# Kernel optimization log

Hardware: AMD Instinct MI355X
Metric: run time of the kernel (lower is better)

The kernel has to match this reference:

```python
import jax, jax.numpy as jnp
import numpy as np

PQ_M = 8
VALS_PER_DIM = 256
SUB_DIM = 64
EMB = PQ_M * SUB_DIM  # 512
NUM_ITEMS = 1_000_000
BATCH = 256
SEQ = 512


def setup_inputs() -> dict:
    key = jax.random.key(0)
    k1, k2, k3 = jax.random.split(key, 3)
    input_ids = jax.random.randint(k1, (BATCH, SEQ), 0, NUM_ITEMS, dtype=jnp.int64 if jax.config.jax_enable_x64 else jnp.int32).astype(jnp.int32)
    item_codes = jax.random.randint(k2, (NUM_ITEMS, PQ_M), 0, VALS_PER_DIM, dtype=jnp.int32)
    centroids = jax.random.normal(k3, (PQ_M, VALS_PER_DIM, SUB_DIM), dtype=jnp.float32)
    # module zeroes centroid index 0 in every subspace at init
    centroids = centroids.at[:, 0, :].set(0.0)
    return {"input_ids": input_ids, "item_codes": item_codes, "centroids": centroids}


def reference(input_ids, item_codes, centroids):
    # input_ids: [B, S] int; item_codes: [N, M] int32; centroids: [M, V, D] f32
    codes = item_codes[input_ids]                       # [B, S, M]
    codes = jnp.minimum(codes, VALS_PER_DIM - 1)        # clamp per subspace
    byte_idx = jnp.arange(PQ_M, dtype=jnp.int32)        # [M]
    # per-subspace gather: centroids[m, codes[b,s,m]] -> [B, S, M, D]
    sub = centroids[byte_idx[None, None, :], codes]
    B, S = input_ids.shape
    result = sub.reshape(B, S, EMB)                     # concat subspaces
    pad = (input_ids == 0)[:, :, None]                  # zero padding tokens
    return jnp.where(pad, 0.0, result)
```

## Files before the change

kernel.cpp:

```cpp
#include <hip/hip_runtime.h>


#define PQ_M_ 8
#define VALS_ 256
#define SUB_ 64
#define NTOK_ (256 * 512)
#define TOK_PER_BLK 64
#define THREADS 256

typedef float f4 __attribute__((ext_vector_type(4)));

__global__ __launch_bounds__(THREADS) void ItemCode_kernel(
    const int* __restrict__ input_ids,
    const int* __restrict__ item_codes,
    const float* __restrict__ centroids,
    float* __restrict__ out)
{
    __shared__ int s_cidx[TOK_PER_BLK * PQ_M_];

    const int tok_base = blockIdx.x * TOK_PER_BLK;

    #pragma unroll
    for (int k = threadIdx.x; k < TOK_PER_BLK * PQ_M_; k += THREADS) {
        const int t  = k >> 3;
        const int m  = k & 7;
        const int id = input_ids[tok_base + t];
        int code = 0;
        if (id != 0) {
            code = __builtin_nontemporal_load(&item_codes[id * PQ_M_ + m]);
            code = min(code, VALS_ - 1);
        }
        s_cidx[k] = ((m * VALS_) + code) << 4;
    }
    __syncthreads();

    const f4* __restrict__ cent4 = reinterpret_cast<const f4*>(centroids);
    f4* __restrict__ out4 = reinterpret_cast<f4*>(out);
    const int out_base = tok_base * 128;

    #pragma unroll 8
    for (int i = threadIdx.x; i < TOK_PER_BLK * 128; i += THREADS) {
        const int t   = i >> 7;
        const int e   = i & 127;
        const int m   = e >> 4;
        const int s4  = e & 15;
        const int ci  = s_cidx[(t << 3) | m] + s4;
        const f4 v = cent4[ci];
        __builtin_nontemporal_store(v, &out4[out_base + i]);
    }
}

extern "C" void kernel_launch(void* const* d_in, const int* in_sizes, int n_in,
                              void* d_out, int out_size, void* d_ws, size_t ws_size,
                              hipStream_t stream) {
    const int*   input_ids  = (const int*)d_in[0];
    const int*   item_codes = (const int*)d_in[1];
    const float* centroids  = (const float*)d_in[2];
    float*       out        = (float*)d_out;

    dim3 grid(NTOK_ / TOK_PER_BLK), block(THREADS);
    ItemCode_kernel<<<grid, block, 0, stream>>>(input_ids, item_codes, centroids, out);
}
```

Before: 58.82 us.

## Double-buffer code staging in chunks to overlap index gather with output writes

Splits each block's 64 tokens into four chunks of 16. Half the threads prefetch the next chunk's item codes into registers while all threads write the current chunk's centroid rows, using a ping-pong shared buffer. The aim is to hide the dependent id→code gather latency behind the output stores. The cost is a barrier per chunk, and only 128 threads issue the random item_codes loads. It also loads item_codes unconditionally, including row 0 for padding tokens.

```diff
diff --git a/kernel.cpp b/kernel.cpp
--- a/kernel.cpp
+++ b/kernel.cpp
@@ -1,12 +1,13 @@
 #include <hip/hip_runtime.h>
 
 
-#define PQ_M_ 8
 #define VALS_ 256
-#define SUB_ 64
 #define NTOK_ (256 * 512)
-#define TOK_PER_BLK 64
+#define TOKS_BLK 64
+#define TOK_CHUNK 16
+#define CHUNKS (TOKS_BLK / TOK_CHUNK)
 #define THREADS 256
+#define ITERS (TOK_CHUNK * 128 / THREADS)
 
 typedef float f4 __attribute__((ext_vector_type(4)));
 
@@ -16,37 +17,51 @@
     const float* __restrict__ centroids,
     float* __restrict__ out)
 {
-    __shared__ int s_cidx[TOK_PER_BLK * PQ_M_];
+    __shared__ int s_cidx[2][TOK_CHUNK * 8];
 
-    const int tok_base = blockIdx.x * TOK_PER_BLK;
+    const int tid = threadIdx.x;
+    const int blk_tok0 = blockIdx.x * TOKS_BLK;
 
-    #pragma unroll
-    for (int k = threadIdx.x; k < TOK_PER_BLK * PQ_M_; k += THREADS) {
-        const int t  = k >> 3;
-        const int m  = k & 7;
-        const int id = input_ids[tok_base + t];
-        int code = 0;
-        if (id != 0) {
-            code = __builtin_nontemporal_load(&item_codes[id * PQ_M_ + m]);
-            code = min(code, VALS_ - 1);
-        }
-        s_cidx[k] = ((m * VALS_) + code) << 4;
-    }
-    __syncthreads();
+    const int pt = tid >> 3;
+    const int pm = tid & 7;
+    const bool stager = (tid < TOK_CHUNK * 8);
+
+    const int e  = tid & 127;
+    const int m  = e >> 4;
+    const int s4 = e & 15;
+    const int t0 = tid >> 7;
 
     const f4* __restrict__ cent4 = reinterpret_cast<const f4*>(centroids);
     f4* __restrict__ out4 = reinterpret_cast<f4*>(out);
-    const int out_base = tok_base * 128;
 
-    #pragma unroll 8
-    for (int i = threadIdx.x; i < TOK_PER_BLK * 128; i += THREADS) {
-        const int t   = i >> 7;
-        const int e   = i & 127;
-        const int m   = e >> 4;
-        const int s4  = e & 15;
-        const int ci  = s_cidx[(t << 3) | m] + s4;
-        const f4 v = cent4[ci];
-        __builtin_nontemporal_store(v, &out4[out_base + i]);
+    auto gather = [&](int c) -> int {
+        const int id = input_ids[blk_tok0 + c * TOK_CHUNK + pt];
+        int code = __builtin_nontemporal_load(&item_codes[id * 8 + pm]);
+        code = min(code, VALS_ - 1);
+        code = (id == 0) ? 0 : code;
+        return ((pm << 8) + code) << 4;
+    };
+
+    int reg;
+    if (stager) {
+        reg = gather(0);
+        s_cidx[0][tid] = reg;
+    }
+
+    for (int c = 0; c < CHUNKS; ++c) {
+        __syncthreads();
+        const bool more = (c + 1 < CHUNKS);
+        if (more && stager) reg = gather(c + 1);
+
+        const int buf = c & 1;
+        const int ob = (blk_tok0 + c * TOK_CHUNK) * 128;
+        #pragma unroll
+        for (int it = 0; it < ITERS; ++it) {
+            const int t  = t0 + it * 2;
+            const int ci = s_cidx[buf][(t << 3) | m] + s4;
+            __builtin_nontemporal_store(cent4[ci], &out4[ob + tid + it * THREADS]);
+        }
+        if (more && stager) s_cidx[buf ^ 1][tid] = reg;
     }
 }
 
@@ -58,6 +73,6 @@
     const float* centroids  = (const float*)d_in[2];
     float*       out        = (float*)d_out;
 
-    dim3 grid(NTOK_ / TOK_PER_BLK), block(THREADS);
+    dim3 grid(NTOK_ / TOKS_BLK), block(THREADS);
     ItemCode_kernel<<<grid, block, 0, stream>>>(input_ids, item_codes, centroids, out);
 }
```

Result: slower. 63.65 us (+8.2%).

## Stage per-subspace centroid table in LDS and split blocks by subspace

Applied to the files above, without the earlier changes.

Each block now handles one PQ subspace for a 512-token chunk and copies that subspace's 256x64 centroid table into shared memory. Outputs are then gathered from LDS instead of global memory. This is meant to cut random global/L2 gather traffic. In exchange, every block reloads 64 KB of table, occupancy drops because of the large LDS footprint, and output stores become 256-byte strided segments.

```diff
diff --git a/kernel.cpp b/kernel.cpp
--- a/kernel.cpp
+++ b/kernel.cpp
@@ -1,12 +1,11 @@
 #include <hip/hip_runtime.h>
 
 
-#define PQ_M_ 8
 #define VALS_ 256
-#define SUB_ 64
 #define NTOK_ (256 * 512)
-#define TOK_PER_BLK 64
+#define T_BLK 512
 #define THREADS 256
+#define ROWS_F4 16
 
 typedef float f4 __attribute__((ext_vector_type(4)));
 
@@ -16,37 +15,42 @@
     const float* __restrict__ centroids,
     float* __restrict__ out)
 {
-    __shared__ int s_cidx[TOK_PER_BLK * PQ_M_];
+    __shared__ f4  s_tab[VALS_ * ROWS_F4];
+    __shared__ int s_off[T_BLK];
 
-    const int tok_base = blockIdx.x * TOK_PER_BLK;
+    const int bid   = blockIdx.x;
+    const int m     = bid & 7;
+    const int chunk = bid >> 3;
+    const int tid   = threadIdx.x;
+    const int tok0  = chunk * T_BLK;
+
+    const f4* __restrict__ cent4 =
+        reinterpret_cast<const f4*>(centroids) + m * (VALS_ * ROWS_F4);
+
+    const int id0 = input_ids[tok0 + tid];
+    const int id1 = input_ids[tok0 + THREADS + tid];
 
     #pragma unroll
-    for (int k = threadIdx.x; k < TOK_PER_BLK * PQ_M_; k += THREADS) {
-        const int t  = k >> 3;
-        const int m  = k & 7;
-        const int id = input_ids[tok_base + t];
-        int code = 0;
-        if (id != 0) {
-            code = __builtin_nontemporal_load(&item_codes[id * PQ_M_ + m]);
-            code = min(code, VALS_ - 1);
-        }
-        s_cidx[k] = ((m * VALS_) + code) << 4;
-    }
+    for (int k = 0; k < ROWS_F4; ++k)
+        s_tab[k * THREADS + tid] = cent4[k * THREADS + tid];
+
+    int c0 = min(__builtin_nontemporal_load(&item_codes[id0 * 8 + m]), VALS_ - 1);
+    int c1 = min(__builtin_nontemporal_load(&item_codes[id1 * 8 + m]), VALS_ - 1);
+    s_off[tid]           = (id0 ? c0 : 0) << 4;
+    s_off[tid + THREADS] = (id1 ? c1 : 0) << 4;
+
     __syncthreads();
 
-    const f4* __restrict__ cent4 = reinterpret_cast<const f4*>(centroids);
+    const int t_lo = tid >> 4;
+    const int s4   = tid & 15;
     f4* __restrict__ out4 = reinterpret_cast<f4*>(out);
-    const int out_base = tok_base * 128;
+    const int obase = (tok0 + t_lo) * 128 + m * 16 + s4;
 
     #pragma unroll 8
-    for (int i = threadIdx.x; i < TOK_PER_BLK * 128; i += THREADS) {
-        const int t   = i >> 7;
-        const int e   = i & 127;
-        const int m   = e >> 4;
-        const int s4  = e & 15;
-        const int ci  = s_cidx[(t << 3) | m] + s4;
-        const f4 v = cent4[ci];
-        __builtin_nontemporal_store(v, &out4[out_base + i]);
+    for (int it = 0; it < T_BLK / 16; ++it) {
+        const int tl = it * 16 + t_lo;
+        const f4 v = s_tab[s_off[tl] + s4];
+        __builtin_nontemporal_store(v, &out4[obase + it * (16 * 128)]);
     }
 }
 
@@ -58,6 +62,6 @@
     const float* centroids  = (const float*)d_in[2];
     float*       out        = (float*)d_out;
 
-    dim3 grid(NTOK_ / TOK_PER_BLK), block(THREADS);
+    dim3 grid(8 * (NTOK_ / T_BLK)), block(THREADS);
     ItemCode_kernel<<<grid, block, 0, stream>>>(input_ids, item_codes, centroids, out);
 }
```

New measurement: 81.95 us. 1.39x slower.
